# Kernel tuning notes

Measured on AMD Instinct MI355X. Metric: run time of the kernel, lower is better.

The kernel has to match this reference:

```python
import jax, jax.numpy as jnp
import numpy as np

D_X = D_Z = D_ATTN = D_OUT = 2048
L_Z = 32768


def setup_inputs() -> dict:
    key = jax.random.key(0)
    ks = jax.random.split(key, 8)
    xavier_q = (2.0 / (D_X + D_ATTN)) ** 0.5
    xavier_k = (2.0 / (D_Z + D_ATTN)) ** 0.5
    xavier_v = (2.0 / (D_Z + D_OUT)) ** 0.5
    return {
        "x": jax.random.normal(ks[0], (D_X,), jnp.float32),
        "zs": jax.random.normal(ks[1], (L_Z, D_Z), jnp.float32),
        "x_mask": 1,
        "zs_mask": jax.random.randint(ks[2], (L_Z,), 0, 2, jnp.int64.dtype if jax.config.read('jax_enable_x64') else jnp.int32),
        "w_q": jax.random.normal(ks[3], (D_X, D_ATTN), jnp.float32) * xavier_q,
        "w_k": jax.random.normal(ks[4], (D_Z, D_ATTN), jnp.float32) * xavier_k,
        "w_v": jax.random.normal(ks[5], (D_Z, D_OUT), jnp.float32) * xavier_v,
        "b_q": jnp.zeros((D_ATTN,), jnp.float32),
        "b_k": jnp.zeros((D_ATTN,), jnp.float32),
        "b_v": jnp.zeros((D_OUT,), jnp.float32),
    }


def reference(x, zs, x_mask, zs_mask, w_q, w_k, w_v, b_q, b_k, b_v):
    scale = 1.0 / jnp.sqrt(jnp.asarray(w_q.shape[1], x.dtype))
    q = x @ w_q + b_q                       # [d_attn]
    k = zs @ w_k + b_k                      # [l_z, d_attn]
    v = zs @ w_v + b_v                      # [l_z, d_out]
    score = (k @ q) * scale                 # [l_z]
    mask = (x_mask * zs_mask).astype(score.dtype)  # [l_z]
    bmask = mask != 0
    neg = jnp.finfo(score.dtype).min
    masked_score = jnp.where(bmask, score, neg)
    attention = jax.nn.softmax(masked_score, axis=-1) * mask  # [l_z]
    vt = attention @ v                      # [d_out] (vectorized form of the python loop)
    return (q, k, v, score, mask, masked_score, attention, vt)
```

## Files before the change

### kernel.cpp

```cpp
#include <hip/hip_runtime.h>
#include <hip/hip_bf16.h>
#include <cfloat>

#define DD   2048
#define LZ   32768

#define NEG_SENTINEL (-3.3895313892515355e38f)

typedef __bf16          bf16x8   __attribute__((ext_vector_type(8)));
typedef float           f32x4    __attribute__((ext_vector_type(4)));
typedef unsigned short  ushort8v __attribute__((ext_vector_type(8)));
typedef unsigned short  ushort4v __attribute__((ext_vector_type(4)));
typedef unsigned short  ushort_t;

typedef __attribute__((address_space(1))) const unsigned int guint_t;
typedef __attribute__((address_space(3))) unsigned int       luint_t;

__device__ __forceinline__ void gload16(const void* g, void* l) {
    __builtin_amdgcn_global_load_lds((guint_t*)g, (luint_t*)l, 16, 0, 0);
}

__device__ __forceinline__ unsigned short bf16_rne(float x) {
    unsigned u = __builtin_bit_cast(unsigned, x);
    u += 0x7fffu + ((u >> 16) & 1u);
    return (unsigned short)(u >> 16);
}

__device__ __forceinline__ void split_bf16(float x, unsigned short& hi, unsigned short& lo) {
    unsigned u = __builtin_bit_cast(unsigned, x);
    hi = (unsigned short)(u >> 16);
    float r = x - __builtin_bit_cast(float, u & 0xffff0000u);
    unsigned v = __builtin_bit_cast(unsigned, r);
    v += 0x7fffu + ((v >> 16) & 1u);
    lo = (unsigned short)(v >> 16);
}

#define TILE_US 8192

__global__ __launch_bounds__(256) void init_qvt(const float* __restrict__ b_q,
                                                float* __restrict__ q,
                                                float* __restrict__ vt) {
    int i = blockIdx.x * 256 + threadIdx.x;
    q[i]  = b_q[i];
    vt[i] = 0.0f;
}

__global__ __launch_bounds__(256) void q_gemv(const float* __restrict__ x,
                                              const float* __restrict__ w_q,
                                              float* __restrict__ q) {
    int n  = blockIdx.x * 256 + threadIdx.x;
    int c0 = blockIdx.y * 128;
    float acc = 0.0f;
    for (int c = 0; c < 128; ++c)
        acc = fmaf(x[c0 + c], w_q[(size_t)(c0 + c) * DD + n], acc);
    atomicAdd(&q[n], acc);
}

__global__ __launch_bounds__(256) void prea_kernel(const float* __restrict__ zs,
                                                   ushort_t* __restrict__ a_ws) {
    const int T = blockIdx.x;
    const int p = blockIdx.y;
    const int t = threadIdx.x;
    ushort_t* tile = a_ws + ((size_t)p * 32 + T) * TILE_US;
    #pragma unroll
    for (int j = 0; j < 4; ++j) {
        const int idx = t + j * 256;
        const int row = idx >> 3, k8 = idx & 7;
        const float4* src = (const float4*)(zs + ((size_t)p * 128 + row) * DD + T * 64 + k8 * 8);
        float4 f0 = src[0], f1 = src[1];
        ushort8v hv;
        hv[0] = bf16_rne(f0.x); hv[1] = bf16_rne(f0.y);
        hv[2] = bf16_rne(f0.z); hv[3] = bf16_rne(f0.w);
        hv[4] = bf16_rne(f1.x); hv[5] = bf16_rne(f1.y);
        hv[6] = bf16_rne(f1.z); hv[7] = bf16_rne(f1.w);
        const int phys = k8 ^ (row & 7);
        *(ushort8v*)(tile + (row * 8 + phys) * 8) = hv;
    }
}

__global__ __launch_bounds__(256) void preb_kernel(const float* __restrict__ w_k,
                                                   const float* __restrict__ w_v,
                                                   ushort_t* __restrict__ b_ws) {
    __shared__ float tile[64][65];
    const int mat = blockIdx.z;
    const float* w = mat ? w_v : w_k;
    const int T = blockIdx.x;
    const int kt0 = T * 64, nt0 = blockIdx.y * 64;
    const int t = threadIdx.x;
    const int rl  = t >> 4;
    const int cl4 = (t & 15) * 4;
    #pragma unroll
    for (int j = 0; j < 4; ++j) {
        float4 v4 = *(const float4*)&w[(size_t)(kt0 + rl + j * 16) * DD + nt0 + cl4];
        tile[rl + j * 16][cl4 + 0] = v4.x;
        tile[rl + j * 16][cl4 + 1] = v4.y;
        tile[rl + j * 16][cl4 + 2] = v4.z;
        tile[rl + j * 16][cl4 + 3] = v4.w;
    }
    __syncthreads();
    #pragma unroll
    for (int jj = 0; jj < 2; ++jj) {
        const int idx = t + jj * 256;
        const int n_l = idx >> 3, k8 = idx & 7;
        const int ng    = mat * DD + nt0 + n_l;
        const int panel = ng >> 7, prow = ng & 127;
        ushort8v hv;
        #pragma unroll
        for (int e = 0; e < 8; ++e)
            hv[e] = bf16_rne(tile[k8 * 8 + e][n_l]);
        ushort_t* dst = b_ws + ((size_t)panel * 32 + T) * TILE_US;
        const int phys = k8 ^ (prow & 7);
        *(ushort8v*)(dst + (prow * 8 + phys) * 8) = hv;
    }
}

__device__ __forceinline__ void vm_wait8() { asm volatile("s_waitcnt vmcnt(8)" ::: "memory"); }
__device__ __forceinline__ void vm_wait0() { asm volatile("s_waitcnt vmcnt(0)" ::: "memory"); }

__device__ __forceinline__ void kv_stage(const ushort_t* __restrict__ a_blk,
                                         const ushort_t* __restrict__ b_blk,
                                         char* LdsA, char* LdsB,
                                         int T, int wid, int lane) {
    const int p = T & 1;
    const bool isA = wid < 4;
    const int w4 = isA ? wid : wid - 4;
    const int h = w4 >> 1, qr = w4 & 1;
    const ushort_t* src = (isA ? a_blk : b_blk) + ((size_t)h * 32 + T) * TILE_US + qr * 4096;
    char* dst = (isA ? LdsA : LdsB) + p * 32768 + h * 16384 + qr * 8192;
    #pragma unroll
    for (int i = 0; i < 8; ++i) {
        const int g = i * 64 + lane;
        gload16(src + (size_t)g * 8, dst + g * 16);
    }
}

#define CLUSTER(AF, BF, R0)                                                              \
    {                                                                                    \
        _Pragma("unroll")                                                                \
        for (int i2 = 0; i2 < 4; ++i2) {                                                 \
            _Pragma("unroll")                                                            \
            for (int j = 0; j < 4; ++j)                                                  \
                acc[(R0) + i2][j] = __builtin_amdgcn_mfma_f32_16x16x32_bf16(             \
                    AF[i2], BF[j], acc[(R0) + i2][j], 0, 0, 0);                          \
        }                                                                                \
    }

#define LD8(dst, base, off)                                                              \
    dst = __builtin_bit_cast(bf16x8, *(const ushort8v*)((base) + (off)));

#define LGKM(N)  asm volatile("s_waitcnt lgkmcnt(" #N ")" ::: "memory")

template<int TAIL>
__device__ __forceinline__ void kv_iter(
    const ushort_t* __restrict__ a_blk, const ushort_t* __restrict__ b_blk,
    char* LdsA, char* LdsB, int T,
    int wid, int lane, int wm, int wn,
    int soh, int sol, int arow, int brow,
    bf16x8 (&a0)[4], bf16x8 (&b0)[4],
    f32x4 (&acc)[8][4])
{
    const int p = T & 1;
    const char* Ab = LdsA + p * 32768 + wm * 16384;
    const char* Bb = LdsB + p * 32768 + (wn >> 1) * 16384;

    bf16x8 a1[4], a2[4], a3[4], b1[4];

    #pragma unroll
    for (int i = 0; i < 4; ++i) LD8(a1[i], Ab, arow + (4 + i) * 2048 + soh);
    #pragma unroll
    for (int i = 0; i < 4; ++i) LD8(a2[i], Ab, arow + i * 2048 + sol);
    LGKM(8);
    __builtin_amdgcn_sched_barrier(0);
    __builtin_amdgcn_s_setprio(1);
    CLUSTER(a0, b0, 0);
    __builtin_amdgcn_s_setprio(0);

    #pragma unroll
    for (int i = 0; i < 4; ++i) LD8(a3[i], Ab, arow + (4 + i) * 2048 + sol);
    #pragma unroll
    for (int j = 0; j < 4; ++j) LD8(b1[j], Bb, brow + j * 2048 + sol);
    LGKM(8);
    __builtin_amdgcn_sched_barrier(0);
    __builtin_amdgcn_s_setprio(1);
    CLUSTER(a1, b0, 4);
    __builtin_amdgcn_s_setprio(0);

    LGKM(0);
    __builtin_amdgcn_sched_barrier(0);
    __builtin_amdgcn_s_barrier();

    if (TAIL == 0) kv_stage(a_blk, b_blk, LdsA, LdsB, T + 2, wid, lane);
    __builtin_amdgcn_sched_barrier(0);
    __builtin_amdgcn_s_setprio(1);
    CLUSTER(a2, b1, 0);
    __builtin_amdgcn_s_setprio(0);

    if (TAIL == 0) vm_wait8();
    if (TAIL == 1) vm_wait0();
    __builtin_amdgcn_sched_barrier(0);
    __builtin_amdgcn_s_barrier();

    if (TAIL <= 1) {
        const int np = (T + 1) & 1;
        const char* Abn = LdsA + np * 32768 + wm * 16384;
        const char* Bbn = LdsB + np * 32768 + (wn >> 1) * 16384;
        #pragma unroll
        for (int i = 0; i < 4; ++i) LD8(a0[i], Abn, arow + i * 2048 + soh);
        #pragma unroll
        for (int j = 0; j < 4; ++j) LD8(b0[j], Bbn, brow + j * 2048 + soh);
    }
    __builtin_amdgcn_sched_barrier(0);
    __builtin_amdgcn_s_setprio(1);
    CLUSTER(a3, b1, 4);
    __builtin_amdgcn_s_setprio(0);
}

__global__ __launch_bounds__(512, 2)
void kv_gemm256(const ushort_t* __restrict__ a_ws, const ushort_t* __restrict__ b_ws,
                const float* __restrict__ b_k, const float* __restrict__ b_v,
                float* __restrict__ out_k, float* __restrict__ out_v)
{
    __shared__ char LdsA[2 * 32768];
    __shared__ char LdsB[2 * 32768];

    const int tid  = threadIdx.x;
    const int wid  = tid >> 6;
    const int lane = tid & 63;
    const int wm   = wid >> 2;
    const int wn   = wid & 3;
    const int lrow = lane & 15;
    const int lq   = lane >> 4;

    const int lin = blockIdx.x;
    const int swz = (lin & 7) * 256 + (lin >> 3);
    const int nb  = swz & 15;
    const int mb  = swz >> 4;

    const int m0   = mb * 256;
    const int n0   = nb * 256;
    const int mat  = n0 >> 11;
    const int nloc = n0 & (DD - 1);

    const ushort_t* a_blk = a_ws + (size_t)(mb * 2) * 32 * TILE_US;
    const ushort_t* b_blk = b_ws + (size_t)(nb * 2) * 32 * TILE_US;

    const int soh  = ((lq       ^ (lrow & 7)) << 4);
    const int sol  = (((lq | 4) ^ (lrow & 7)) << 4);
    const int arow = lrow * 128;
    const int brow = (wn & 1) * 8192 + lrow * 128;

    f32x4 acc[8][4] = {};
    bf16x8 a0[4], b0[4];

    kv_stage(a_blk, b_blk, LdsA, LdsB, 0, wid, lane);
    kv_stage(a_blk, b_blk, LdsA, LdsB, 1, wid, lane);
    vm_wait8();
    __builtin_amdgcn_sched_barrier(0);
    __builtin_amdgcn_s_barrier();
    {
        const char* Ab0 = LdsA + wm * 16384;
        const char* Bb0 = LdsB + (wn >> 1) * 16384;
        #pragma unroll
        for (int i = 0; i < 4; ++i) LD8(a0[i], Ab0, arow + i * 2048 + soh);
        #pragma unroll
        for (int j = 0; j < 4; ++j) LD8(b0[j], Bb0, brow + j * 2048 + soh);
    }

    for (int T = 0; T < 30; ++T)
        kv_iter<0>(a_blk, b_blk, LdsA, LdsB, T, wid, lane, wm, wn,
                   soh, sol, arow, brow, a0, b0, acc);
    kv_iter<1>(a_blk, b_blk, LdsA, LdsB, 30, wid, lane, wm, wn,
               soh, sol, arow, brow, a0, b0, acc);
    kv_iter<2>(a_blk, b_blk, LdsA, LdsB, 31, wid, lane, wm, wn,
               soh, sol, arow, brow, a0, b0, acc);

    const float* bias = mat ? b_v : b_k;
    float* outp = mat ? out_v : out_k;
    const int lq4 = lq * 4;
    #pragma unroll
    for (int j = 0; j < 4; ++j) {
        const int nout = nloc + wn * 64 + j * 16 + lrow;
        const float bv = bias[nout];
        #pragma unroll
        for (int i = 0; i < 8; ++i) {
            const int mbase = m0 + wm * 128 + i * 16 + lq4;
            #pragma unroll
            for (int r = 0; r < 4; ++r)
                outp[(size_t)(mbase + r) * DD + nout] = acc[i][j][r] + bv;
        }
    }
}

__global__ __launch_bounds__(256)
void kv_gemm_fb(const float* __restrict__ zs,
                const float* __restrict__ w_k, const float* __restrict__ w_v,
                const float* __restrict__ b_k, const float* __restrict__ b_v,
                float* __restrict__ out_k, float* __restrict__ out_v)
{
    __shared__ ushort_t As[128 * 64];
    __shared__ ushort_t Bs[128 * 64];

    const int tid  = threadIdx.x;
    const int m0   = blockIdx.y * 128;
    const int n0   = blockIdx.x * 128;
    const int mat  = n0 >> 11;
    const int nloc = n0 & (DD - 1);

    const int wid  = tid >> 6;
    const int lane = tid & 63;
    const int wm   = wid >> 1;
    const int wn   = wid & 1;
    const int lrow = lane & 15;
    const int lq   = lane >> 4;

    int aoff_hi[4], aoff_lo[4], boff_hi[4], boff_lo[4];
    #pragma unroll
    for (int i = 0; i < 4; ++i) {
        const int ra = wm * 64 + i * 16 + lrow;
        aoff_hi[i] = ra * 128 + ((lq       ^ (ra & 7)) * 16);
        aoff_lo[i] = ra * 128 + (((lq + 4) ^ (ra & 7)) * 16);
        const int rb = wn * 64 + i * 16 + lrow;
        boff_hi[i] = rb * 128 + ((lq       ^ (rb & 7)) * 16);
        boff_lo[i] = rb * 128 + (((lq + 4) ^ (rb & 7)) * 16);
    }

    f32x4 acc[4][4] = {};
    const int srow  = tid >> 1;
    const int shalf = tid & 1;

    for (int ks = 0; ks < 64; ++ks) {
        {
            const float4* ap = (const float4*)(zs + (size_t)(m0 + srow) * DD + ks * 32 + shalf * 16);
            float4 f0 = ap[0], f1 = ap[1], f2 = ap[2], f3 = ap[3];
            float e[16] = {f0.x,f0.y,f0.z,f0.w, f1.x,f1.y,f1.z,f1.w,
                           f2.x,f2.y,f2.z,f2.w, f3.x,f3.y,f3.z,f3.w};
            ushort8v h0, h1, l0, l1;
            #pragma unroll
            for (int c = 0; c < 8; ++c) {
                unsigned short hh, ll;
                split_bf16(e[c], hh, ll);
                h0[c] = hh; l0[c] = ll;
                split_bf16(e[8 + c], hh, ll);
                h1[c] = hh; l1[c] = ll;
            }
            char* rowbase = (char*)As + srow * 128;
            const int s0 = (shalf * 2)     ^ (srow & 7);
            const int s1 = (shalf * 2 + 1) ^ (srow & 7);
            *(ushort8v*)(rowbase + s0 * 16)       = h0;
            *(ushort8v*)(rowbase + s1 * 16)       = h1;
            *(ushort8v*)(rowbase + (s0 ^ 4) * 16) = l0;
            *(ushort8v*)(rowbase + (s1 ^ 4) * 16) = l1;
        }
        {
            const float* w = mat ? w_v : w_k;
            const int k_l = (tid >> 5) * 4;
            const int n_l = (tid & 31) * 4;
            float4 r0 = *(const float4*)&w[(size_t)(ks * 32 + k_l + 0) * DD + nloc + n_l];
            float4 r1 = *(const float4*)&w[(size_t)(ks * 32 + k_l + 1) * DD + nloc + n_l];
            float4 r2 = *(const float4*)&w[(size_t)(ks * 32 + k_l + 2) * DD + nloc + n_l];
            float4 r3 = *(const float4*)&w[(size_t)(ks * 32 + k_l + 3) * DD + nloc + n_l];
            float el[4][4] = {{r0.x,r0.y,r0.z,r0.w},{r1.x,r1.y,r1.z,r1.w},
                              {r2.x,r2.y,r2.z,r2.w},{r3.x,r3.y,r3.z,r3.w}};
            const int slot = k_l >> 3, sub = ((k_l >> 2) & 1) * 8;
            #pragma unroll
            for (int c = 0; c < 4; ++c) {
                const int n = n_l + c;
                ushort4v hv, lv;
                #pragma unroll
                for (int r = 0; r < 4; ++r) {
                    unsigned short hh, ll;
                    split_bf16(el[r][c], hh, ll);
                    hv[r] = hh; lv[r] = ll;
                }
                char* rb = (char*)Bs + n * 128;
                const int sp = slot ^ (n & 7);
                *(ushort4v*)(rb + sp * 16 + sub)       = hv;
                *(ushort4v*)(rb + (sp ^ 4) * 16 + sub) = lv;
            }
        }
        __syncthreads();

        bf16x8 a_hi[4], a_lo[4], b_hi[4], b_lo[4];
        #pragma unroll
        for (int i = 0; i < 4; ++i) {
            a_hi[i] = __builtin_bit_cast(bf16x8, *(const ushort8v*)((const char*)As + aoff_hi[i]));
            a_lo[i] = __builtin_bit_cast(bf16x8, *(const ushort8v*)((const char*)As + aoff_lo[i]));
            b_hi[i] = __builtin_bit_cast(bf16x8, *(const ushort8v*)((const char*)Bs + boff_hi[i]));
            b_lo[i] = __builtin_bit_cast(bf16x8, *(const ushort8v*)((const char*)Bs + boff_lo[i]));
        }
        #pragma unroll
        for (int i = 0; i < 4; ++i)
            #pragma unroll
            for (int j = 0; j < 4; ++j)
                acc[i][j] = __builtin_amdgcn_mfma_f32_16x16x32_bf16(a_hi[i], b_hi[j], acc[i][j], 0, 0, 0);
        #pragma unroll
        for (int i = 0; i < 4; ++i)
            #pragma unroll
            for (int j = 0; j < 4; ++j)
                acc[i][j] = __builtin_amdgcn_mfma_f32_16x16x32_bf16(a_hi[i], b_lo[j], acc[i][j], 0, 0, 0);
        #pragma unroll
        for (int i = 0; i < 4; ++i)
            #pragma unroll
            for (int j = 0; j < 4; ++j)
                acc[i][j] = __builtin_amdgcn_mfma_f32_16x16x32_bf16(a_lo[i], b_hi[j], acc[i][j], 0, 0, 0);
        __syncthreads();
    }

    const float* bias = mat ? b_v : b_k;
    float* outp = mat ? out_v : out_k;
    #pragma unroll
    for (int j = 0; j < 4; ++j) {
        const int nout = nloc + wn * 64 + j * 16 + lrow;
        const float bv = bias[nout];
        #pragma unroll
        for (int i = 0; i < 4; ++i) {
            const int mbase = m0 + wm * 64 + i * 16 + lq * 4;
            #pragma unroll
            for (int r = 0; r < 4; ++r)
                outp[(size_t)(mbase + r) * DD + nout] = acc[i][j][r] + bv;
        }
    }
}

__global__ __launch_bounds__(256) void score_kernel(const float* __restrict__ k,
                                                    const float* __restrict__ q,
                                                    const int* __restrict__ x_mask,
                                                    const int* __restrict__ zs_mask,
                                                    float* __restrict__ score,
                                                    float* __restrict__ maskout,
                                                    float* __restrict__ masked) {
    const int wid = threadIdx.x >> 6, lane = threadIdx.x & 63;
    const int l = blockIdx.x * 4 + wid;
    const float4* krow = (const float4*)(k + (size_t)l * DD);
    const float4* q4   = (const float4*)q;
    float acc = 0.0f;
    #pragma unroll
    for (int it = 0; it < 8; ++it) {
        float4 kv = krow[lane + it * 64];
        float4 qv = q4[lane + it * 64];
        acc = fmaf(kv.x, qv.x, acc);
        acc = fmaf(kv.y, qv.y, acc);
        acc = fmaf(kv.z, qv.z, acc);
        acc = fmaf(kv.w, qv.w, acc);
    }
    #pragma unroll
    for (int off = 32; off; off >>= 1) acc += __shfl_xor(acc, off, 64);
    if (lane == 0) {
        float s = acc * 0.022097086912079608f;
        float m = (float)(x_mask[0] * zs_mask[l]);
        score[l]   = s;
        maskout[l] = m;
        masked[l]  = (m != 0.0f) ? s : NEG_SENTINEL;
    }
}

__global__ __launch_bounds__(1024) void softmax_kernel(const float* __restrict__ masked,
                                                       const float* __restrict__ maskv,
                                                       float* __restrict__ attention) {
    __shared__ float red[16];
    __shared__ float gsh[2];
    const int t = threadIdx.x;
    const int wid = t >> 6, lane = t & 63;

    float mx = -FLT_MAX;
    for (int i = t; i < LZ; i += 1024) mx = fmaxf(mx, masked[i]);
    #pragma unroll
    for (int off = 32; off; off >>= 1) mx = fmaxf(mx, __shfl_xor(mx, off, 64));
    if (lane == 0) red[wid] = mx;
    __syncthreads();
    if (t == 0) {
        float g = red[0];
        for (int i = 1; i < 16; ++i) g = fmaxf(g, red[i]);
        gsh[0] = g;
    }
    __syncthreads();
    const float gmax = gsh[0];

    float s = 0.0f;
    for (int i = t; i < LZ; i += 1024) s += expf(masked[i] - gmax);
    #pragma unroll
    for (int off = 32; off; off >>= 1) s += __shfl_xor(s, off, 64);
    if (lane == 0) red[wid] = s;
    __syncthreads();
    if (t == 0) {
        float g = 0.0f;
        for (int i = 0; i < 16; ++i) g += red[i];
        gsh[1] = g;
    }
    __syncthreads();
    const float inv = 1.0f / gsh[1];

    for (int i = t; i < LZ; i += 1024)
        attention[i] = expf(masked[i] - gmax) * inv * maskv[i];
}

__global__ __launch_bounds__(256) void vt_kernel(const float* __restrict__ v,
                                                 const float* __restrict__ attention,
                                                 float* __restrict__ vt) {
    __shared__ float att_s[512];
    const int t = threadIdx.x;
    const int d = blockIdx.x * 256 + t;
    const int l0 = blockIdx.y * 512;
    att_s[t]       = attention[l0 + t];
    att_s[t + 256] = attention[l0 + t + 256];
    __syncthreads();
    float acc = 0.0f;
    const float* vp = v + (size_t)l0 * DD + d;
    for (int i = 0; i < 512; ++i)
        acc = fmaf(att_s[i], vp[(size_t)i * DD], acc);
    atomicAdd(&vt[d], acc);
}

extern "C" void kernel_launch(void* const* d_in, const int* in_sizes, int n_in,
                              void* d_out, int out_size, void* d_ws, size_t ws_size,
                              hipStream_t stream) {
    const float* x       = (const float*)d_in[0];
    const float* zs      = (const float*)d_in[1];
    const int*   x_mask  = (const int*)d_in[2];
    const int*   zs_mask = (const int*)d_in[3];
    const float* w_q     = (const float*)d_in[4];
    const float* w_k     = (const float*)d_in[5];
    const float* w_v     = (const float*)d_in[6];
    const float* b_q     = (const float*)d_in[7];
    const float* b_k     = (const float*)d_in[8];
    const float* b_v     = (const float*)d_in[9];

    float* out       = (float*)d_out;
    float* q         = out;
    float* k         = q + DD;
    float* v         = k + (size_t)LZ * DD;
    float* score     = v + (size_t)LZ * DD;
    float* maskv     = score + LZ;
    float* masked    = maskv + LZ;
    float* attention = masked + LZ;
    float* vt        = attention + LZ;

    init_qvt<<<8, 256, 0, stream>>>(b_q, q, vt);
    q_gemv<<<dim3(8, 16), 256, 0, stream>>>(x, w_q, q);

    const size_t A_WS = (size_t)256 * 32 * TILE_US * sizeof(ushort_t);
    const size_t B_WS = (size_t)32  * 32 * TILE_US * sizeof(ushort_t);

    if (ws_size >= A_WS + B_WS) {
        ushort_t* a_ws = (ushort_t*)d_ws;
        ushort_t* b_ws = (ushort_t*)((char*)d_ws + A_WS);
        prea_kernel<<<dim3(32, 256), 256, 0, stream>>>(zs, a_ws);
        preb_kernel<<<dim3(32, 32, 2), 256, 0, stream>>>(w_k, w_v, b_ws);
        kv_gemm256<<<2048, 512, 0, stream>>>(a_ws, b_ws, b_k, b_v, k, v);
    } else {
        kv_gemm_fb<<<dim3(32, 256), 256, 0, stream>>>(zs, w_k, w_v, b_k, b_v, k, v);
    }

    score_kernel<<<8192, 256, 0, stream>>>(k, q, x_mask, zs_mask, score, maskv, masked);
    softmax_kernel<<<1, 1024, 0, stream>>>(masked, maskv, attention);
    vt_kernel<<<dim3(8, 64), 256, 0, stream>>>(v, attention, vt);
}
```

Measured before the change: 800.5 us.

## Fuse attention score dot product into K GEMM epilogue and fuse softmax prep

Computes k·q partial sums in the K GEMM epilogue from the register accumulators and reduces them via shuffles and atomics into a raw score buffer, zeroed in the pre-conversion kernel. This removes the separate pass that rereads the full K matrix. The softmax kernel now applies scale and mask, writes score/mask/masked, and keeps values in registers instead of rereading them. It adds atomics and extra epilogue work to the GEMM, and changes the summation order of the scores.

```diff
diff --git a/kernel.cpp b/kernel.cpp
--- a/kernel.cpp
+++ b/kernel.cpp
@@ -4,6 +4,7 @@
 
 #define DD   2048
 #define LZ   32768
+#define SCALE_Q 0.022097086912079608f
 
 #define NEG_SENTINEL (-3.3895313892515355e38f)
 
@@ -57,10 +58,12 @@
 }
 
 __global__ __launch_bounds__(256) void prea_kernel(const float* __restrict__ zs,
-                                                   ushort_t* __restrict__ a_ws) {
+                                                   ushort_t* __restrict__ a_ws,
+                                                   float* __restrict__ raw) {
     const int T = blockIdx.x;
     const int p = blockIdx.y;
     const int t = threadIdx.x;
+    if (T == 0 && t < 128) raw[p * 128 + t] = 0.0f;
     ushort_t* tile = a_ws + ((size_t)p * 32 + T) * TILE_US;
     #pragma unroll
     for (int j = 0; j < 4; ++j) {
@@ -218,6 +221,7 @@
 __global__ __launch_bounds__(512, 2)
 void kv_gemm256(const ushort_t* __restrict__ a_ws, const ushort_t* __restrict__ b_ws,
                 const float* __restrict__ b_k, const float* __restrict__ b_v,
+                const float* __restrict__ qvec, float* __restrict__ raw,
                 float* __restrict__ out_k, float* __restrict__ out_v)
 {
     __shared__ char LdsA[2 * 32768];
@@ -277,16 +281,40 @@
     const float* bias = mat ? b_v : b_k;
     float* outp = mat ? out_v : out_k;
     const int lq4 = lq * 4;
+    float bv[4], qv[4];
     #pragma unroll
     for (int j = 0; j < 4; ++j) {
         const int nout = nloc + wn * 64 + j * 16 + lrow;
-        const float bv = bias[nout];
+        bv[j] = bias[nout];
+        qv[j] = qvec[nout];
+    }
+    #pragma unroll
+    for (int j = 0; j < 4; ++j) {
+        const int nout = nloc + wn * 64 + j * 16 + lrow;
         #pragma unroll
         for (int i = 0; i < 8; ++i) {
             const int mbase = m0 + wm * 128 + i * 16 + lq4;
             #pragma unroll
             for (int r = 0; r < 4; ++r)
-                outp[(size_t)(mbase + r) * DD + nout] = acc[i][j][r] + bv;
+                outp[(size_t)(mbase + r) * DD + nout] = acc[i][j][r] + bv[j];
+        }
+    }
+    if (mat == 0) {
+        #pragma unroll
+        for (int i = 0; i < 8; ++i) {
+            #pragma unroll
+            for (int r = 0; r < 4; ++r) {
+                float psum = 0.0f;
+                #pragma unroll
+                for (int j = 0; j < 4; ++j)
+                    psum = fmaf(acc[i][j][r] + bv[j], qv[j], psum);
+                psum += __shfl_xor(psum, 1);
+                psum += __shfl_xor(psum, 2);
+                psum += __shfl_xor(psum, 4);
+                psum += __shfl_xor(psum, 8);
+                if (lrow == 0)
+                    atomicAdd(&raw[m0 + wm * 128 + i * 16 + lq4 + r], psum);
+            }
         }
     }
 }
@@ -422,13 +450,9 @@
     }
 }
 
-__global__ __launch_bounds__(256) void score_kernel(const float* __restrict__ k,
-                                                    const float* __restrict__ q,
-                                                    const int* __restrict__ x_mask,
-                                                    const int* __restrict__ zs_mask,
-                                                    float* __restrict__ score,
-                                                    float* __restrict__ maskout,
-                                                    float* __restrict__ masked) {
+__global__ __launch_bounds__(256) void score_raw_kernel(const float* __restrict__ k,
+                                                        const float* __restrict__ q,
+                                                        float* __restrict__ raw) {
     const int wid = threadIdx.x >> 6, lane = threadIdx.x & 63;
     const int l = blockIdx.x * 4 + wid;
     const float4* krow = (const float4*)(k + (size_t)l * DD);
@@ -445,25 +469,35 @@
     }
     #pragma unroll
     for (int off = 32; off; off >>= 1) acc += __shfl_xor(acc, off, 64);
-    if (lane == 0) {
-        float s = acc * 0.022097086912079608f;
-        float m = (float)(x_mask[0] * zs_mask[l]);
-        score[l]   = s;
-        maskout[l] = m;
-        masked[l]  = (m != 0.0f) ? s : NEG_SENTINEL;
-    }
-}
-
-__global__ __launch_bounds__(1024) void softmax_kernel(const float* __restrict__ masked,
-                                                       const float* __restrict__ maskv,
-                                                       float* __restrict__ attention) {
+    if (lane == 0) raw[l] = acc;
+}
+
+__global__ __launch_bounds__(1024) void softmax_fused(const int* __restrict__ x_mask,
+                                                      const int* __restrict__ zs_mask,
+                                                      float* __restrict__ score,
+                                                      float* __restrict__ maskv,
+                                                      float* __restrict__ masked,
+                                                      float* __restrict__ attention) {
     __shared__ float red[16];
     __shared__ float gsh[2];
     const int t = threadIdx.x;
     const int wid = t >> 6, lane = t & 63;
-
+    const float xm = (float)x_mask[0];
+
+    float msv[32];
     float mx = -FLT_MAX;
-    for (int i = t; i < LZ; i += 1024) mx = fmaxf(mx, masked[i]);
+    #pragma unroll
+    for (int c = 0; c < 32; ++c) {
+        const int i = t + c * 1024;
+        const float s  = masked[i] * SCALE_Q;
+        const float m  = xm * (float)zs_mask[i];
+        const float ms = (m != 0.0f) ? s : NEG_SENTINEL;
+        score[i]  = s;
+        maskv[i]  = m;
+        masked[i] = ms;
+        msv[c] = ms;
+        mx = fmaxf(mx, ms);
+    }
     #pragma unroll
     for (int off = 32; off; off >>= 1) mx = fmaxf(mx, __shfl_xor(mx, off, 64));
     if (lane == 0) red[wid] = mx;
@@ -477,7 +511,12 @@
     const float gmax = gsh[0];
 
     float s = 0.0f;
-    for (int i = t; i < LZ; i += 1024) s += expf(masked[i] - gmax);
+    #pragma unroll
+    for (int c = 0; c < 32; ++c) {
+        const float e = expf(msv[c] - gmax);
+        msv[c] = e;
+        s += e;
+    }
     #pragma unroll
     for (int off = 32; off; off >>= 1) s += __shfl_xor(s, off, 64);
     if (lane == 0) red[wid] = s;
@@ -490,8 +529,12 @@
     __syncthreads();
     const float inv = 1.0f / gsh[1];
 
-    for (int i = t; i < LZ; i += 1024)
-        attention[i] = expf(masked[i] - gmax) * inv * maskv[i];
+    #pragma unroll
+    for (int c = 0; c < 32; ++c) {
+        const int i = t + c * 1024;
+        const float m = xm * (float)zs_mask[i];
+        attention[i] = msv[c] * inv * m;
+    }
 }
 
 __global__ __launch_bounds__(256) void vt_kernel(const float* __restrict__ v,
@@ -544,14 +587,14 @@
     if (ws_size >= A_WS + B_WS) {
         ushort_t* a_ws = (ushort_t*)d_ws;
         ushort_t* b_ws = (ushort_t*)((char*)d_ws + A_WS);
-        prea_kernel<<<dim3(32, 256), 256, 0, stream>>>(zs, a_ws);
+        prea_kernel<<<dim3(32, 256), 256, 0, stream>>>(zs, a_ws, masked);
         preb_kernel<<<dim3(32, 32, 2), 256, 0, stream>>>(w_k, w_v, b_ws);
-        kv_gemm256<<<2048, 512, 0, stream>>>(a_ws, b_ws, b_k, b_v, k, v);
+        kv_gemm256<<<2048, 512, 0, stream>>>(a_ws, b_ws, b_k, b_v, q, masked, k, v);
     } else {
         kv_gemm_fb<<<dim3(32, 256), 256, 0, stream>>>(zs, w_k, w_v, b_k, b_v, k, v);
-    }
-
-    score_kernel<<<8192, 256, 0, stream>>>(k, q, x_mask, zs_mask, score, maskv, masked);
-    softmax_kernel<<<1, 1024, 0, stream>>>(masked, maskv, attention);
+        score_raw_kernel<<<8192, 256, 0, stream>>>(k, q, masked);
+    }
+
+    softmax_fused<<<1, 1024, 0, stream>>>(x_mask, zs_mask, score, maskv, masked, attention);
     vt_kernel<<<dim3(8, 64), 256, 0, stream>>>(v, attention, vt);
 }
```

New measurement: 787.8 us. No clear change (-1.6%).
